# Kernel optimization log

Measured on AMD Instinct MI355X. Metric: run time of the kernel, lower is better.

The kernel has to match this reference:

```python
import jax, jax.numpy as jnp
import numpy as np
import math

NUM_HEADS = 16
HEAD_DIM = 64
DIM = 1024
IO_SLOTS = 16
NEG_INF = 1.0e9


def _alibi_slopes(num_heads):
    # slopes = ratio**i for i in 1..n, ratio = 2**(-8/n)
    ratio = 2.0 ** (-8.0 / num_heads)
    return jnp.array([ratio ** i for i in range(1, num_heads + 1)], dtype=jnp.float32)


def setup_inputs() -> dict:
    key = jax.random.key(0)
    ks = jax.random.split(key, 7)
    B, S, D = 2, 2048, DIM
    x = jax.random.normal(ks[0], (B, S, D), dtype=jnp.float32)
    is_getchar = jax.random.uniform(ks[1], (B, S), dtype=jnp.float32)
    is_putchar = jax.random.uniform(ks[2], (B, S), dtype=jnp.float32)
    scale = 0.02
    wq = jax.random.normal(ks[3], (D, NUM_HEADS * HEAD_DIM), dtype=jnp.float32) * scale
    wk = jax.random.normal(ks[4], (D, NUM_HEADS * HEAD_DIM), dtype=jnp.float32) * scale
    wv = jax.random.normal(ks[5], (D, NUM_HEADS * HEAD_DIM), dtype=jnp.float32) * scale
    wo = jax.random.normal(ks[6], (NUM_HEADS * HEAD_DIM, D), dtype=jnp.float32) * scale
    return {"x": x, "is_getchar": is_getchar, "is_putchar": is_putchar,
            "wq": wq, "wk": wk, "wv": wv, "wo": wo}


def reference(x, is_getchar, is_putchar, wq, wk, wv, wo):
    B, S, D = x.shape
    H, hd = NUM_HEADS, HEAD_DIM
    io_start = D - IO_SLOTS

    q = (x @ wq).reshape(B, S, H, hd)
    k = (x @ wk).reshape(B, S, H, hd)
    v = (x @ wv).reshape(B, S, H, hd)

    # scores[b,h,i,j] = q . k / sqrt(hd)
    scores = jnp.einsum("bihd,bjhd->bhij", q, k) / math.sqrt(hd)

    # standard ALiBi bias: -slope * (i - j), causal masked
    positions = jnp.arange(S)
    dist = (positions[:, None] - positions[None, :]).astype(jnp.float32)  # [S,S] = i - j
    slopes = _alibi_slopes(H)  # [H]
    bias = -slopes[:, None, None] * dist  # [H,S,S]
    causal = jnp.triu(jnp.ones((S, S), dtype=jnp.float32), k=1)
    bias = bias - causal * NEG_INF
    scores = scores + bias[None]

    # targeted read-head bias on head 0: -slope0 * |target - j|
    read_anchor = x[..., io_start + 0]  # [B,S]
    read_offset = x[..., io_start + 1]  # [B,S]
    target = read_anchor + 1.0 + read_offset  # [B,S]
    read_bias = -slopes[0] * jnp.abs(target[..., None] - positions.astype(jnp.float32))  # [B,S,S]
    head0 = jnp.where(is_getchar[:, None, :, None] > 0.5, read_bias[:, None], scores[:, :1])
    scores = scores.at[:, :1].set(head0)

    attn = jax.nn.softmax(scores, axis=-1)
    attn_out = jnp.einsum("bhij,bjhd->bihd", attn, v).reshape(B, S, H * hd)
    output = x + attn_out @ wo

    # I/O state updates (last 16 channels)
    output = output.at[..., io_start + 1].add(is_getchar)   # read_offset += getchar
    output = output.at[..., io_start + 3].add(is_putchar)   # write_offset += putchar
    output = output.at[..., io_start + 13].set(is_putchar)  # output_ready = putchar
    return output
```

## Files before the change

kernel.cpp:

```cpp
#include <hip/hip_runtime.h>
#include <hip/hip_bf16.h>

typedef __hip_bfloat16 bf16;
typedef __attribute__((ext_vector_type(8))) short short8;
typedef __attribute__((ext_vector_type(4))) short short4v;
typedef __attribute__((ext_vector_type(4))) float f32x4;

#define MFMA16(a, b, c) __builtin_amdgcn_mfma_f32_16x16x32_bf16((a), (b), (c), 0, 0, 0)

#if __has_builtin(__builtin_amdgcn_mfma_f32_16x16x16bf16_1k)
#define MFMA_PV(a, b, c) __builtin_amdgcn_mfma_f32_16x16x16bf16_1k((a), (b), (c), 0, 0, 0)
#elif __has_builtin(__builtin_amdgcn_mfma_f32_16x16x16_bf16)
#define MFMA_PV(a, b, c) __builtin_amdgcn_mfma_f32_16x16x16_bf16((a), (b), (c), 0, 0, 0)
#else
static __device__ __forceinline__ f32x4 mfma_pv_asm(short4v a, short4v b, f32x4 c) {
    f32x4 d;
    asm volatile("v_mfma_f32_16x16x16_bf16 %0, %1, %2, %3"
                 : "=&v"(d) : "v"(a), "v"(b), "v"(c));
    return d;
}
#define MFMA_PV(a, b, c) mfma_pv_asm((a), (b), (c))
#endif

static __device__ __forceinline__ void gload_lds16(const bf16* g, bf16* l) {
    __builtin_amdgcn_global_load_lds((const __attribute__((address_space(1))) void*)g,
                                     (__attribute__((address_space(3))) void*)l, 16, 0, 0);
}

__global__ __launch_bounds__(256) void prep_kernel(
    const float* __restrict__ x,
    const float* __restrict__ wq, const float* __restrict__ wk,
    const float* __restrict__ wv, const float* __restrict__ wo,
    bf16* __restrict__ Xb, bf16* __restrict__ WqkvT, bf16* __restrict__ WoT) {
    __shared__ bf16 tile[64][65];
    int bid = blockIdx.x;
    if (bid < 4096) {
        int i = (bid * 256 + threadIdx.x) * 4;
        float4 v = *(const float4*)(x + i);
        union { bf16 h4[4]; uint2 u; } p;
        p.h4[0] = __float2bfloat16(v.x);
        p.h4[1] = __float2bfloat16(v.y);
        p.h4[2] = __float2bfloat16(v.z);
        p.h4[3] = __float2bfloat16(v.w);
        *(uint2*)(Xb + i) = p.u;
        return;
    }
    int t2 = bid - 4096;
    int mat = t2 >> 8;
    int t   = t2 & 255;
    int tn  = t >> 4, tk = t & 15;
    const float* src = (mat == 0) ? wq : (mat == 1) ? wk : (mat == 2) ? wv : wo;
    bf16* dst = (mat < 3) ? (WqkvT + (size_t)mat * 1024 * 1024) : WoT;
    int tx = threadIdx.x & 63, ty = threadIdx.x >> 6;
    int k0 = tk * 64, n0 = tn * 64;
#pragma unroll
    for (int p = 0; p < 16; ++p) {
        int r = p * 4 + ty;
        tile[r][tx] = __float2bfloat16(src[(size_t)(k0 + r) * 1024 + n0 + tx]);
    }
    __syncthreads();
#pragma unroll
    for (int p = 0; p < 16; ++p) {
        int r = p * 4 + ty;
        dst[(size_t)(n0 + r) * 1024 + k0 + tx] = tile[tx][r];
    }
}

__global__ __launch_bounds__(256) void gemm_qkv_kernel(
    const bf16* __restrict__ A, const bf16* __restrict__ Bt,
    bf16* __restrict__ QK, bf16* __restrict__ Vt) {
    const int K = 1024;
    int bm = blockIdx.x, bn = blockIdx.y;
    __shared__ bf16 As[128 * 32];
    __shared__ bf16 Bs[128 * 32];
    int tid = threadIdx.x;
    int lane = tid & 63, w = tid >> 6;
    int wm = (w >> 1) * 64, wn = (w & 1) * 64;
    int q4 = lane >> 4, li = lane & 15;
    int srow = tid >> 2, sc = (tid & 3) * 8;

    const bf16* Ag = A + (size_t)(bm * 128 + srow) * K + sc;
    const bf16* Bg = Bt + (size_t)(bn * 128 + srow) * K + sc;
    bf16* Asl = As + tid * 8;
    bf16* Asl2 = As + 2048 + tid * 8;
    bf16* Bsl = Bs + tid * 8;
    bf16* Bsl2 = Bs + 2048 + tid * 8;

    f32x4 acc[4][4];
#pragma unroll
    for (int mt = 0; mt < 4; ++mt)
#pragma unroll
        for (int nt = 0; nt < 4; ++nt) acc[mt][nt] = (f32x4){0.f, 0.f, 0.f, 0.f};

    for (int k0 = 0; k0 < K; k0 += 32) {
        __syncthreads();
        gload_lds16(Ag + k0, Asl);
        gload_lds16(Ag + 64 * K + k0, Asl2);
        gload_lds16(Bg + k0, Bsl);
        gload_lds16(Bg + 64 * K + k0, Bsl2);
        __syncthreads();
        short8 af[4], bfb[4];
#pragma unroll
        for (int mt = 0; mt < 4; ++mt)
            af[mt] = *(const short8*)(As + (wm + mt * 16 + li) * 32 + q4 * 8);
#pragma unroll
        for (int nt = 0; nt < 4; ++nt)
            bfb[nt] = *(const short8*)(Bs + (wn + nt * 16 + li) * 32 + q4 * 8);
#pragma unroll
        for (int mt = 0; mt < 4; ++mt)
#pragma unroll
            for (int nt = 0; nt < 4; ++nt)
                acc[mt][nt] = MFMA16(af[mt], bfb[nt], acc[mt][nt]);
    }

    int rowb = bm * 128 + wm;
    if (bn < 16) {
        float qs = (bn < 8) ? 0.1803368801111244f : 1.0f;
#pragma unroll
        for (int mt = 0; mt < 4; ++mt) {
#pragma unroll
            for (int nt = 0; nt < 4; ++nt) {
                int col = bn * 128 + wn + nt * 16 + li;
#pragma unroll
                for (int r = 0; r < 4; ++r) {
                    int row = rowb + mt * 16 + q4 * 4 + r;
                    QK[(size_t)row * 2048 + col] = __float2bfloat16(acc[mt][nt][r] * qs);
                }
            }
        }
    } else {
#pragma unroll
        for (int mt = 0; mt < 4; ++mt) {
            int sbase = rowb + mt * 16 + q4 * 4;
            int b = sbase >> 11, s = sbase & 2047;
#pragma unroll
            for (int nt = 0; nt < 4; ++nt) {
                int n = bn * 128 + wn + nt * 16 + li - 2048;
                int h = n >> 6, d = n & 63;
                union { bf16 h4[4]; uint2 u; } pk;
#pragma unroll
                for (int r = 0; r < 4; ++r) pk.h4[r] = __float2bfloat16(acc[mt][nt][r]);
                *(uint2*)(Vt + (size_t)((b * 16 + h) * 64 + d) * 2048 + s) = pk.u;
            }
        }
    }
}

__global__ __launch_bounds__(256, 3) void attn_kernel(
    const bf16* __restrict__ QK, const bf16* __restrict__ Vt,
    const float* __restrict__ x, const float* __restrict__ gch,
    bf16* __restrict__ AO) {
    const int S = 2048;
    int idx = blockIdx.x;
    int ti, h, b;
    if (idx < 64) { h = 0; b = idx & 1; ti = idx >> 1; }
    else {
        int i2 = idx - 64;
        int row = i2 / 30;
        int j = i2 - row * 30;
        ti = 31 - row; h = 1 + (j >> 1); b = j & 1;
    }
    int i0 = ti * 64;
    int tid = threadIdx.x, lane = tid & 63, w = tid >> 6;
    int q4 = lane >> 4, li = lane & 15;

    __shared__ __align__(16) char smem[36864];
    bf16* Ks0 = (bf16*)(smem);
    bf16* Ks1 = (bf16*)(smem + 9216);
    bf16* Vs0 = (bf16*)(smem + 18432);
    bf16* Vs1 = (bf16*)(smem + 27648);
    float* Ored  = (float*)(smem);
    float* lsumB = (float*)(smem + 17408);

    short8 qf[4][2];
#pragma unroll
    for (int it = 0; it < 4; ++it) {
        const bf16* qp = QK + (size_t)(b * S + i0 + it * 16 + li) * 2048 + h * 64 + q4 * 8;
        qf[it][0] = *(const short8*)(qp);
        qf[it][1] = *(const short8*)(qp + 32);
    }

    const float L2E = 1.4426950408889634f;
    float sl1 = exp2f(-0.5f * (float)(h + 1)) * L2E;
    const float slope0L = 0.70710678118654752f * L2E;

    float tgt[4]; int gcm[4];
    if (h == 0) {
#pragma unroll
        for (int it = 0; it < 4; ++it) {
            size_t ix = (size_t)(b * S + i0 + it * 16 + li);
            gcm[it] = gch[ix] > 0.5f ? 1 : 0;
            tgt[it] = x[ix * 1024 + 1008] + 1.0f + x[ix * 1024 + 1009];
        }
    } else {
#pragma unroll
        for (int it = 0; it < 4; ++it) { gcm[it] = 0; tgt[it] = 0.f; }
    }

    float lsum[4] = {0.f, 0.f, 0.f, 0.f};
    f32x4 o[4][4];
#pragma unroll
    for (int it = 0; it < 4; ++it)
#pragma unroll
        for (int dt = 0; dt < 4; ++dt) o[it][dt] = (f32x4){0.f, 0.f, 0.f, 0.f};

    int srow = tid >> 3, scv = (tid & 7) * 8;
    const bf16* Kg = QK + (size_t)(b * S + srow) * 2048 + 1024 + h * 64 + scv;
    const bf16* Vg = Vt + (size_t)((b * 16 + h) * 64 + srow) * 2048 + scv;

    int ntiles = (h == 0) ? (S / 64) : (ti + 1);

    uint4 kv0 = *(const uint4*)(Kg);
    uint4 kv1 = *(const uint4*)(Kg + (size_t)32 * 2048);
    uint4 vv0 = *(const uint4*)(Vg);
    uint4 vv1 = *(const uint4*)(Vg + (size_t)32 * 2048);
    *(uint4*)(Ks0 + srow * 72 + scv) = kv0;
    *(uint4*)(Ks0 + (srow + 32) * 72 + scv) = kv1;
    *(uint4*)(Vs0 + srow * 72 + scv) = vv0;
    *(uint4*)(Vs0 + (srow + 32) * 72 + scv) = vv1;
    if (ntiles > 1) {
        kv0 = *(const uint4*)(Kg + (size_t)64 * 2048);
        kv1 = *(const uint4*)(Kg + (size_t)96 * 2048);
        vv0 = *(const uint4*)(Vg + 64);
        vv1 = *(const uint4*)(Vg + (size_t)32 * 2048 + 64);
    }
    __syncthreads();

    for (int jt = 0; jt < ntiles; ++jt) {
        const bf16* Kc = (jt & 1) ? Ks1 : Ks0;
        const bf16* Vc = (jt & 1) ? Vs1 : Vs0;
        if (jt + 1 < ntiles) {
            bf16* Kn = (jt & 1) ? Ks0 : Ks1;
            bf16* Vn = (jt & 1) ? Vs0 : Vs1;
            *(uint4*)(Kn + srow * 72 + scv) = kv0;
            *(uint4*)(Kn + (srow + 32) * 72 + scv) = kv1;
            *(uint4*)(Vn + srow * 72 + scv) = vv0;
            *(uint4*)(Vn + (srow + 32) * 72 + scv) = vv1;
            if (jt + 2 < ntiles) {
                size_t jn = (size_t)(jt + 2) * 64;
                kv0 = *(const uint4*)(Kg + jn * 2048);
                kv1 = *(const uint4*)(Kg + (jn + 32) * 2048);
                vv0 = *(const uint4*)(Vg + jn);
                vv1 = *(const uint4*)(Vg + (size_t)32 * 2048 + jn);
            }
        }

        int j0 = jt * 64;
        short8 kf0 = *(const short8*)(Kc + (w * 16 + li) * 72 + q4 * 8);
        short8 kf1 = *(const short8*)(Kc + (w * 16 + li) * 72 + 32 + q4 * 8);
        f32x4 sA[4];
#pragma unroll
        for (int it = 0; it < 4; ++it) {
            f32x4 z = (f32x4){0.f, 0.f, 0.f, 0.f};
            z = MFMA16(kf0, qf[it][0], z);
            z = MFMA16(kf1, qf[it][1], z);
            sA[it] = z;
        }

        float jbase = (float)(j0 + w * 16 + q4 * 4);
        bool diag = (jt >= ti);
        short4v pf[4];
#pragma unroll
        for (int it = 0; it < 4; ++it) {
            float fi = (float)(i0 + it * 16 + li);
            float d0 = jbase - fi;
            union { bf16 hh[4]; short4v v; } pu;
#pragma unroll
            for (int r = 0; r < 4; ++r) {
                float dj = d0 + (float)r;
                float p;
                if (h == 0) {
                    float s = fmaf(sl1, dj, sA[it][r]);
                    float sg = -slope0L * fabsf(tgt[it] - (jbase + (float)r));
                    s = gcm[it] ? sg : s;
                    p = exp2f(s);
                    if (!gcm[it] && dj > 0.f) p = 0.f;
                } else {
                    float s = fmaf(sl1, dj, sA[it][r]);
                    p = exp2f(s);
                    if (diag && dj > 0.f) p = 0.f;
                }
                lsum[it] += p;
                pu.hh[r] = __float2bfloat16(p);
            }
            pf[it] = pu.v;
        }

#pragma unroll
        for (int dt = 0; dt < 4; ++dt) {
            short4v vf = *(const short4v*)(Vc + (dt * 16 + li) * 72 + w * 16 + q4 * 4);
#pragma unroll
            for (int it = 0; it < 4; ++it)
                o[it][dt] = MFMA_PV(pf[it], vf, o[it][dt]);
        }
        __syncthreads();
    }

#pragma unroll
    for (int it = 0; it < 4; ++it) {
        lsum[it] += __shfl_xor(lsum[it], 16, 64);
        lsum[it] += __shfl_xor(lsum[it], 32, 64);
    }
    if (lane < 16) {
#pragma unroll
        for (int it = 0; it < 4; ++it) lsumB[w * 64 + it * 16 + lane] = lsum[it];
    }

    __syncthreads();
    if (w == 0) {
#pragma unroll
        for (int it = 0; it < 4; ++it)
#pragma unroll
            for (int dt = 0; dt < 4; ++dt)
#pragma unroll
                for (int r = 0; r < 4; ++r)
                    Ored[(it * 16 + q4 * 4 + r) * 68 + dt * 16 + li] = o[it][dt][r];
    }
    __syncthreads();
    if (w == 1) {
#pragma unroll
        for (int it = 0; it < 4; ++it)
#pragma unroll
            for (int dt = 0; dt < 4; ++dt)
#pragma unroll
                for (int r = 0; r < 4; ++r)
                    Ored[(it * 16 + q4 * 4 + r) * 68 + dt * 16 + li] += o[it][dt][r];
    }
    __syncthreads();
    if (w == 2) {
#pragma unroll
        for (int it = 0; it < 4; ++it)
#pragma unroll
            for (int dt = 0; dt < 4; ++dt)
#pragma unroll
                for (int r = 0; r < 4; ++r)
                    Ored[(it * 16 + q4 * 4 + r) * 68 + dt * 16 + li] += o[it][dt][r];
    }
    __syncthreads();
    if (w == 3) {
#pragma unroll
        for (int it = 0; it < 4; ++it)
#pragma unroll
            for (int dt = 0; dt < 4; ++dt)
#pragma unroll
                for (int r = 0; r < 4; ++r)
                    Ored[(it * 16 + q4 * 4 + r) * 68 + dt * 16 + li] += o[it][dt][r];
    }
    __syncthreads();

    int i = tid >> 2, dseg = (tid & 3) * 16;
    float ls = lsumB[i] + lsumB[64 + i] + lsumB[128 + i] + lsumB[192 + i];
    float inv = 1.0f / ls;
    bf16* dst = AO + (size_t)(b * S + i0 + i) * 1024 + h * 64 + dseg;
    union { bf16 hh[16]; uint4 u[2]; } ou;
#pragma unroll
    for (int c = 0; c < 16; ++c)
        ou.hh[c] = __float2bfloat16(Ored[i * 68 + dseg + c] * inv);
    *(uint4*)(dst) = ou.u[0];
    *(uint4*)(dst + 8) = ou.u[1];
}

__global__ __launch_bounds__(256) void gemm_out_kernel(
    const bf16* __restrict__ A, const bf16* __restrict__ Bt,
    const float* __restrict__ x, const float* __restrict__ gch,
    const float* __restrict__ pch, float* __restrict__ out) {
    const int K = 1024;
    int bm = blockIdx.x, bn = blockIdx.y;
    __shared__ bf16 As[128 * 32];
    __shared__ bf16 Bs[128 * 32];
    int tid = threadIdx.x;
    int lane = tid & 63, w = tid >> 6;
    int wm = (w >> 1) * 64, wn = (w & 1) * 64;
    int q4 = lane >> 4, li = lane & 15;
    int srow = tid >> 2, sc = (tid & 3) * 8;

    const bf16* Ag = A + (size_t)(bm * 128 + srow) * K + sc;
    const bf16* Bg = Bt + (size_t)(bn * 128 + srow) * K + sc;
    bf16* Asl = As + tid * 8;
    bf16* Asl2 = As + 2048 + tid * 8;
    bf16* Bsl = Bs + tid * 8;
    bf16* Bsl2 = Bs + 2048 + tid * 8;

    f32x4 acc[4][4];
#pragma unroll
    for (int mt = 0; mt < 4; ++mt)
#pragma unroll
        for (int nt = 0; nt < 4; ++nt) acc[mt][nt] = (f32x4){0.f, 0.f, 0.f, 0.f};

    for (int k0 = 0; k0 < K; k0 += 32) {
        __syncthreads();
        gload_lds16(Ag + k0, Asl);
        gload_lds16(Ag + 64 * K + k0, Asl2);
        gload_lds16(Bg + k0, Bsl);
        gload_lds16(Bg + 64 * K + k0, Bsl2);
        __syncthreads();
        short8 af[4], bfb[4];
#pragma unroll
        for (int mt = 0; mt < 4; ++mt)
            af[mt] = *(const short8*)(As + (wm + mt * 16 + li) * 32 + q4 * 8);
#pragma unroll
        for (int nt = 0; nt < 4; ++nt)
            bfb[nt] = *(const short8*)(Bs + (wn + nt * 16 + li) * 32 + q4 * 8);
#pragma unroll
        for (int mt = 0; mt < 4; ++mt)
#pragma unroll
            for (int nt = 0; nt < 4; ++nt)
                acc[mt][nt] = MFMA16(af[mt], bfb[nt], acc[mt][nt]);
    }

#pragma unroll
    for (int mt = 0; mt < 4; ++mt) {
#pragma unroll
        for (int nt = 0; nt < 4; ++nt) {
            int col = bn * 128 + wn + nt * 16 + li;
#pragma unroll
            for (int r = 0; r < 4; ++r) {
                int row = bm * 128 + wm + mt * 16 + q4 * 4 + r;
                size_t idx = (size_t)row * 1024 + col;
                float v = x[idx] + acc[mt][nt][r];
                if (col == 1009) v += gch[row];
                else if (col == 1011) v += pch[row];
                else if (col == 1021) v = pch[row];
                out[idx] = v;
            }
        }
    }
}

extern "C" void kernel_launch(void* const* d_in, const int* in_sizes, int n_in,
                              void* d_out, int out_size, void* d_ws, size_t ws_size,
                              hipStream_t stream) {
    (void)in_sizes; (void)n_in; (void)out_size; (void)ws_size;
    const float* x   = (const float*)d_in[0];
    const float* gch = (const float*)d_in[1];
    const float* pch = (const float*)d_in[2];
    const float* wq  = (const float*)d_in[3];
    const float* wk  = (const float*)d_in[4];
    const float* wv  = (const float*)d_in[5];
    const float* wo  = (const float*)d_in[6];
    float* out = (float*)d_out;

    char* ws = (char*)d_ws;
    bf16* Xb    = (bf16*)(ws);
    bf16* WqkvT = (bf16*)(ws + (size_t)( 8 << 20));
    bf16* WoT   = (bf16*)(ws + (size_t)(14 << 20));
    bf16* QK    = (bf16*)(ws + (size_t)(16 << 20));
    bf16* Vt    = (bf16*)(ws + (size_t)(32 << 20));
    bf16* AO    = Xb;

    prep_kernel<<<5120, 256, 0, stream>>>(x, wq, wk, wv, wo, Xb, WqkvT, WoT);
    gemm_qkv_kernel<<<dim3(32, 24), 256, 0, stream>>>(Xb, WqkvT, QK, Vt);
    attn_kernel<<<1024, 256, 0, stream>>>(QK, Vt, x, gch, AO);
    gemm_out_kernel<<<dim3(32, 8), 256, 0, stream>>>(AO, WoT, x, gch, pch, out);
}
```

Baseline: 212.2 us.

## Split long attention rows into two KV halves merged via atomic tickets

Query tiles with more than 16 KV tiles (all of head 0, and causal rows with ti≥16) are now handled by two blocks, each covering half of the KV range. The block that takes the first atomic ticket writes its unnormalized partial output (bf16) and row sum to a workspace slot. The second block spin-waits on a release/acquire flag, then merges and normalizes. The aim is to shorten the longest blocks and reduce tail imbalance across the grid. It also raises launch bounds to 4 waves per SIMD, adds a memset, stores the partial output in bf16 (some precision loss), and reuses workspace that overlaps the weight buffer.

```diff
diff --git a/kernel.cpp b/kernel.cpp
--- a/kernel.cpp
+++ b/kernel.cpp
@@ -146,25 +146,41 @@
     }
 }
 
-__global__ __launch_bounds__(256, 3) void attn_kernel(
+__global__ __launch_bounds__(256, 4) void attn_kernel(
     const bf16* __restrict__ QK, const bf16* __restrict__ Vt,
     const float* __restrict__ x, const float* __restrict__ gch,
-    bf16* __restrict__ AO) {
+    bf16* __restrict__ AO, int* __restrict__ cnt, int* __restrict__ done,
+    char* __restrict__ part) {
     const int S = 2048;
     int idx = blockIdx.x;
-    int ti, h, b;
-    if (idx < 64) { h = 0; b = idx & 1; ti = idx >> 1; }
-    else {
-        int i2 = idx - 64;
-        int row = i2 / 30;
-        int j = i2 - row * 30;
-        ti = 31 - row; h = 1 + (j >> 1); b = j & 1;
+    int ti, h, b, jt0, jt1, sid;
+    if (idx < 128) {
+        int u = idx >> 1, c = idx & 1;
+        h = 0; b = u & 1; ti = u >> 1;
+        jt0 = c * 16; jt1 = c ? 32 : 16;
+        sid = u;
+    } else if (idx < 1088) {
+        int v = idx - 128;
+        ti = 31 - v / 60;
+        int g = v % 60;
+        int hb = g >> 1, c = g & 1;
+        h = 1 + (hb >> 1); b = hb & 1;
+        jt0 = c ? 16 : 0; jt1 = c ? (ti + 1) : 16;
+        sid = 64 + (ti - 16) * 30 + hb;
+    } else {
+        int v = idx - 1088;
+        ti = 15 - v / 30;
+        int g = v % 30;
+        h = 1 + (g >> 1); b = g & 1;
+        jt0 = 0; jt1 = ti + 1;
+        sid = -1;
     }
     int i0 = ti * 64;
     int tid = threadIdx.x, lane = tid & 63, w = tid >> 6;
     int q4 = lane >> 4, li = lane & 15;
 
     __shared__ __align__(16) char smem[36864];
+    __shared__ int ticket_sh;
     bf16* Ks0 = (bf16*)(smem);
     bf16* Ks1 = (bf16*)(smem + 9216);
     bf16* Vs0 = (bf16*)(smem + 18432);
@@ -208,36 +224,36 @@
     const bf16* Kg = QK + (size_t)(b * S + srow) * 2048 + 1024 + h * 64 + scv;
     const bf16* Vg = Vt + (size_t)((b * 16 + h) * 64 + srow) * 2048 + scv;
 
-    int ntiles = (h == 0) ? (S / 64) : (ti + 1);
-
-    uint4 kv0 = *(const uint4*)(Kg);
-    uint4 kv1 = *(const uint4*)(Kg + (size_t)32 * 2048);
-    uint4 vv0 = *(const uint4*)(Vg);
-    uint4 vv1 = *(const uint4*)(Vg + (size_t)32 * 2048);
+    int nt_ = jt1 - jt0;
+    size_t g0 = (size_t)jt0 * 64;
+    uint4 kv0 = *(const uint4*)(Kg + g0 * 2048);
+    uint4 kv1 = *(const uint4*)(Kg + (g0 + 32) * 2048);
+    uint4 vv0 = *(const uint4*)(Vg + g0);
+    uint4 vv1 = *(const uint4*)(Vg + (size_t)32 * 2048 + g0);
     *(uint4*)(Ks0 + srow * 72 + scv) = kv0;
     *(uint4*)(Ks0 + (srow + 32) * 72 + scv) = kv1;
     *(uint4*)(Vs0 + srow * 72 + scv) = vv0;
     *(uint4*)(Vs0 + (srow + 32) * 72 + scv) = vv1;
-    if (ntiles > 1) {
-        kv0 = *(const uint4*)(Kg + (size_t)64 * 2048);
-        kv1 = *(const uint4*)(Kg + (size_t)96 * 2048);
-        vv0 = *(const uint4*)(Vg + 64);
-        vv1 = *(const uint4*)(Vg + (size_t)32 * 2048 + 64);
-    }
-    __syncthreads();
-
-    for (int jt = 0; jt < ntiles; ++jt) {
-        const bf16* Kc = (jt & 1) ? Ks1 : Ks0;
-        const bf16* Vc = (jt & 1) ? Vs1 : Vs0;
-        if (jt + 1 < ntiles) {
-            bf16* Kn = (jt & 1) ? Ks0 : Ks1;
-            bf16* Vn = (jt & 1) ? Vs0 : Vs1;
+    if (nt_ > 1) {
+        kv0 = *(const uint4*)(Kg + (g0 + 64) * 2048);
+        kv1 = *(const uint4*)(Kg + (g0 + 96) * 2048);
+        vv0 = *(const uint4*)(Vg + g0 + 64);
+        vv1 = *(const uint4*)(Vg + (size_t)32 * 2048 + g0 + 64);
+    }
+    __syncthreads();
+
+    for (int t = 0; t < nt_; ++t) {
+        const bf16* Kc = (t & 1) ? Ks1 : Ks0;
+        const bf16* Vc = (t & 1) ? Vs1 : Vs0;
+        if (t + 1 < nt_) {
+            bf16* Kn = (t & 1) ? Ks0 : Ks1;
+            bf16* Vn = (t & 1) ? Vs0 : Vs1;
             *(uint4*)(Kn + srow * 72 + scv) = kv0;
             *(uint4*)(Kn + (srow + 32) * 72 + scv) = kv1;
             *(uint4*)(Vn + srow * 72 + scv) = vv0;
             *(uint4*)(Vn + (srow + 32) * 72 + scv) = vv1;
-            if (jt + 2 < ntiles) {
-                size_t jn = (size_t)(jt + 2) * 64;
+            if (t + 2 < nt_) {
+                size_t jn = (size_t)(jt0 + t + 2) * 64;
                 kv0 = *(const uint4*)(Kg + jn * 2048);
                 kv1 = *(const uint4*)(Kg + (jn + 32) * 2048);
                 vv0 = *(const uint4*)(Vg + jn);
@@ -245,6 +261,7 @@
             }
         }
 
+        int jt = jt0 + t;
         int j0 = jt * 64;
         short8 kf0 = *(const short8*)(Kc + (w * 16 + li) * 72 + q4 * 8);
         short8 kf1 = *(const short8*)(Kc + (w * 16 + li) * 72 + 32 + q4 * 8);
@@ -350,14 +367,60 @@
 
     int i = tid >> 2, dseg = (tid & 3) * 16;
     float ls = lsumB[i] + lsumB[64 + i] + lsumB[128 + i] + lsumB[192 + i];
-    float inv = 1.0f / ls;
-    bf16* dst = AO + (size_t)(b * S + i0 + i) * 1024 + h * 64 + dseg;
-    union { bf16 hh[16]; uint4 u[2]; } ou;
-#pragma unroll
-    for (int c = 0; c < 16; ++c)
-        ou.hh[c] = __float2bfloat16(Ored[i * 68 + dseg + c] * inv);
-    *(uint4*)(dst) = ou.u[0];
-    *(uint4*)(dst + 8) = ou.u[1];
+
+    if (sid < 0) {
+        float inv = 1.0f / ls;
+        bf16* dst = AO + (size_t)(b * S + i0 + i) * 1024 + h * 64 + dseg;
+        union { bf16 hh[16]; uint4 u[2]; } ou;
+#pragma unroll
+        for (int c = 0; c < 16; ++c)
+            ou.hh[c] = __float2bfloat16(Ored[i * 68 + dseg + c] * inv);
+        *(uint4*)(dst) = ou.u[0];
+        *(uint4*)(dst + 8) = ou.u[1];
+        return;
+    }
+
+    char* slot = part + (size_t)sid * 8704;
+    bf16* Opart = (bf16*)slot;
+    float* Lpart = (float*)(slot + 8192);
+
+    if (tid == 0) ticket_sh = atomicAdd(&cnt[sid], 1);
+    __syncthreads();
+    int ticket = ticket_sh;
+
+    if (ticket == 0) {
+        union { bf16 hh[16]; uint4 u[2]; } pu;
+#pragma unroll
+        for (int c = 0; c < 16; ++c)
+            pu.hh[c] = __float2bfloat16(Ored[i * 68 + dseg + c]);
+        *(uint4*)(Opart + i * 64 + dseg) = pu.u[0];
+        *(uint4*)(Opart + i * 64 + dseg + 8) = pu.u[1];
+        if ((tid & 3) == 0) Lpart[i] = ls;
+        __threadfence();
+        __syncthreads();
+        if (tid == 0)
+            __hip_atomic_store(&done[sid], 1, __ATOMIC_RELEASE, __HIP_MEMORY_SCOPE_AGENT);
+    } else {
+        if (tid == 0) {
+            while (__hip_atomic_load(&done[sid], __ATOMIC_ACQUIRE, __HIP_MEMORY_SCOPE_AGENT) == 0)
+                __builtin_amdgcn_s_sleep(8);
+        }
+        __syncthreads();
+        float pls = Lpart[i];
+        float inv = 1.0f / (ls + pls);
+        bf16* dst = AO + (size_t)(b * S + i0 + i) * 1024 + h * 64 + dseg;
+        union { bf16 hh[16]; uint4 u[2]; } pv;
+        pv.u[0] = *(const uint4*)(Opart + i * 64 + dseg);
+        pv.u[1] = *(const uint4*)(Opart + i * 64 + dseg + 8);
+        union { bf16 hh[16]; uint4 u[2]; } ou;
+#pragma unroll
+        for (int c = 0; c < 16; ++c) {
+            float v = Ored[i * 68 + dseg + c] + __bfloat162float(pv.hh[c]);
+            ou.hh[c] = __float2bfloat16(v * inv);
+        }
+        *(uint4*)(dst) = ou.u[0];
+        *(uint4*)(dst + 8) = ou.u[1];
+    }
 }
 
 __global__ __launch_bounds__(256) void gemm_out_kernel(
@@ -447,9 +510,13 @@
     bf16* QK    = (bf16*)(ws + (size_t)(16 << 20));
     bf16* Vt    = (bf16*)(ws + (size_t)(32 << 20));
     bf16* AO    = Xb;
+    int*  cnt  = (int*)(ws + (size_t)(8 << 20));
+    int*  done = cnt + 1024;
+    char* part = ws + (size_t)(8 << 20) + 16384;
 
     prep_kernel<<<5120, 256, 0, stream>>>(x, wq, wk, wv, wo, Xb, WqkvT, WoT);
     gemm_qkv_kernel<<<dim3(32, 24), 256, 0, stream>>>(Xb, WqkvT, QK, Vt);
-    attn_kernel<<<1024, 256, 0, stream>>>(QK, Vt, x, gch, AO);
+    hipMemsetAsync(ws + (size_t)(8 << 20), 0, 8192, stream);
+    attn_kernel<<<1568, 256, 0, stream>>>(QK, Vt, x, gch, AO, cnt, done, part);
     gemm_out_kernel<<<dim3(32, 8), 256, 0, stream>>>(AO, WoT, x, gch, pch, out);
 }
```

Measured after the change: 462.7 us. 2.18x slower.
